# Kernel tuning notes

Hardware: AMD Instinct MI355X
Metric: run time of the kernel (lower is better)

Reference implementation:

```python
import jax, jax.numpy as jnp
import numpy as np

T_SEG = 8      # n_segment
K_SIZE = 3     # dynamic temporal kernel size
BN_EPS = 1e-5


def setup_inputs() -> dict:
    key = jax.random.key(0)
    ks = jax.random.split(key, 8)
    B, T, C, H, W = 8, T_SEG, 256, 56, 56
    ch = C // 4          # c_hidden (reduction=4)
    th = T * 2           # t_hidden (temporal_expand=2)
    K = K_SIZE
    f32 = jnp.float32
    return {
        "x": jax.random.normal(ks[0], (B * T, C, H, W), f32),
        "w_spatial": jax.random.normal(ks[1], (1, 2, 7, 7), f32) * 0.05,   # Conv2d(2,1,7)
        "w_reduce": jax.random.normal(ks[2], (ch, C, 3, 1, 1), f32) * 0.02, # Conv3d(C,ch,(3,1,1))
        "bn_gamma": jnp.ones((ch,), f32),
        "bn_beta": jnp.zeros((ch,), f32),
        "bn_mean": jnp.zeros((ch,), f32),
        "bn_var": jnp.ones((ch,), f32),
        "w_expand": jax.random.normal(ks[3], (C, ch, 1, 1, 1), f32) * 0.02, # Conv3d(ch,C,1)
        "w_fc1": jax.random.normal(ks[4], (th, T), f32) * 0.1,
        "b_fc1": jnp.zeros((th,), f32),
        "w_fc2": jax.random.normal(ks[5], (K, th), f32) * 0.1,
        "b_fc2": jnp.zeros((K,), f32).at[K // 2].set(5.0),
    }


def reference(x, w_spatial, w_reduce, bn_gamma, bn_beta, bn_mean, bn_var,
              w_expand, w_fc1, b_fc1, w_fc2, b_fc2):
    T, K = T_SEG, K_SIZE
    BT, C, H, W = x.shape
    B = BT // T

    # ---- spatial SE gate: channel max/mean -> 7x7 conv -> sigmoid ----
    max_c = x.max(axis=1, keepdims=True)                       # (BT,1,H,W)
    avg_c = x.mean(axis=1, keepdims=True)                      # (BT,1,H,W)
    s = jax.lax.conv_general_dilated(
        jnp.concatenate([max_c, avg_c], axis=1), w_spatial,
        window_strides=(1, 1), padding=((3, 3), (3, 3)),
        dimension_numbers=("NCHW", "OIHW", "NCHW"))
    x_s = x * (1.0 + jax.nn.sigmoid(s))                        # (BT,C,H,W)

    # ---- temporal SE gate: conv3d(3,1,1) -> BN -> relu -> 1x1x1 -> sigmoid ----
    x5 = x_s.reshape(B, T, C, H, W).transpose(0, 2, 1, 3, 4)   # (B,C,T,H,W)
    t = jax.lax.conv_general_dilated(
        x5, w_reduce, window_strides=(1, 1, 1),
        padding=((1, 1), (0, 0), (0, 0)),
        dimension_numbers=("NCDHW", "OIDHW", "NCDHW"))         # (B,ch,T,H,W)
    inv = bn_gamma / jnp.sqrt(bn_var + BN_EPS)
    t = jax.nn.relu(t * inv[None, :, None, None, None]
                    + (bn_beta - bn_mean * inv)[None, :, None, None, None])
    t_attn = jax.nn.sigmoid(
        jnp.einsum("oc,bcthw->bothw", w_expand[:, :, 0, 0, 0], t))
    x_t = x5 * (1.0 + t_attn)                                  # (B,C,T,H,W)

    # ---- dynamic per-(batch,channel) temporal kernel ----
    v = x_t.mean(axis=(-2, -1))                                # (B,C,T)
    h = jax.nn.relu(jnp.einsum("bct,ht->bch", v, w_fc1) + b_fc1)
    kernel = jax.nn.softmax(jnp.einsum("bch,kh->bck", h, w_fc2) + b_fc2,
                            axis=-1)                           # (B,C,K)

    # depthwise temporal stencil (groups=B*C conv2d in torch)
    pad = K // 2
    xp = jnp.pad(x_t, ((0, 0), (0, 0), (pad, pad), (0, 0), (0, 0)))
    out = sum(kernel[:, :, k, None, None, None] * xp[:, :, k:k + T]
              for k in range(K))                               # (B,C,T,H,W)

    return out.transpose(0, 2, 1, 3, 4).reshape(BT, C, H, W)
```

## Files before the change

### kernel.cpp

```cpp
#include <hip/hip_runtime.h>
#include <stdint.h>

#define HW 3136
#define Wd 56
#define Cc 256
#define CH 64
#define Tt 8
#define Bb 8
#define VP 49

typedef unsigned short ushort_t;
typedef __attribute__((ext_vector_type(2))) unsigned short us2;
typedef __attribute__((ext_vector_type(4))) unsigned short us4;
typedef __attribute__((ext_vector_type(8))) unsigned short us8;
typedef __attribute__((ext_vector_type(8))) short short8;
typedef __attribute__((ext_vector_type(4))) float f4;
typedef __attribute__((ext_vector_type(2))) float f2;

__device__ __forceinline__ float bf2f(ushort_t u) {
    union { unsigned int i; float f; } v;
    v.i = ((unsigned int)u) << 16;
    return v.f;
}
__device__ __forceinline__ ushort_t f2bf(float f) {
    union { float f; unsigned int i; } v;
    v.f = f;
    unsigned int r = (v.i + 0x7FFFu + ((v.i >> 16) & 1u)) >> 16;
    return (ushort_t)r;
}

__global__ __launch_bounds__(256) void k0_pack(
    const float* __restrict__ wr, const float* __restrict__ bng,
    const float* __restrict__ bnb, const float* __restrict__ bnm,
    const float* __restrict__ bnv, const float* __restrict__ we,
    ushort_t* __restrict__ wpack, ushort_t* __restrict__ wepack,
    float* __restrict__ shb) {
    int bx = blockIdx.x, tid = threadIdx.x;
    if (bx < 24) {
        int dt = bx >> 3, cb = bx & 7;
        int mt = tid >> 6, l = tid & 63;
        int o = mt * 16 + (l & 15);
        float inv = bng[o] * rsqrtf(bnv[o] + 1e-5f);
        int c0 = cb * 32 + (l >> 4) * 8;
        us8 v;
#pragma unroll
        for (int j = 0; j < 8; j++)
            v[j] = f2bf(wr[((long)o * Cc + c0 + j) * 3 + dt] * inv);
        *(us8*)(wpack + (long)bx * 2048 + (mt * 64 + l) * 8) = v;
        if (bx == 0 && tid < CH)
            shb[tid] = bnb[tid] - bnm[tid] * (bng[tid] * rsqrtf(bnv[tid] + 1e-5f));
    } else {
        int u = (bx - 24) * 256 + tid;
        int l = u & 63;
        int c = ((u >> 6) & 15) * 16 + (l & 15);
        int o0 = (u >> 10) * 32 + (l >> 4) * 8;
        us8 v;
#pragma unroll
        for (int j = 0; j < 8; j++)
            v[j] = f2bf(we[(long)c * CH + o0 + j]);
        *(us8*)(wepack + (long)u * 8) = v;
    }
}

__global__ __launch_bounds__(256) void k1_pool(const float* __restrict__ x,
                                               float* __restrict__ pooled) {
    int u = blockIdx.x * 256 + threadIdx.x;
    int px4 = u % 784, bt = u / 784;
    long base = (long)bt * Cc * HW + px4 * 4;
    float mx[4], sm[4];
#pragma unroll
    for (int j = 0; j < 4; j++) { mx[j] = -3.4e38f; sm[j] = 0.f; }
    for (int c = 0; c < Cc; c++) {
        f4 xv = *(const f4*)(x + base + (long)c * HW);
#pragma unroll
        for (int j = 0; j < 4; j++) {
            mx[j] = fmaxf(mx[j], xv[j]);
            sm[j] += xv[j];
        }
    }
    f4 pm, pa;
#pragma unroll
    for (int j = 0; j < 4; j++) { pm[j] = mx[j]; pa[j] = sm[j] * (1.f / 256.f); }
    *(f4*)(pooled + (long)bt * 2 * HW + px4 * 4) = pm;
    *(f4*)(pooled + (long)bt * 2 * HW + HW + px4 * 4) = pa;
}

__global__ __launch_bounds__(256) void k2_conv(const float* __restrict__ pooled,
                                               const float* __restrict__ wsp,
                                               float* __restrict__ gate) {
    __shared__ float img[2 * HW];
    __shared__ float wf[98];
    int bt = blockIdx.x, tid = threadIdx.x;
    const float* src = pooled + (long)bt * 2 * HW;
    for (int i = tid; i < 2 * HW; i += 256) img[i] = src[i];
    if (tid < 98) wf[tid] = wsp[tid];
    __syncthreads();
    for (int p = tid; p < HW; p += 256) {
        int y = p / Wd, xx = p % Wd;
        float acc = 0.f;
        for (int ci = 0; ci < 2; ci++)
            for (int ky = 0; ky < 7; ky++) {
                int yy = y + ky - 3;
                if (yy < 0 || yy >= Wd) continue;
                for (int kx = 0; kx < 7; kx++) {
                    int xc = xx + kx - 3;
                    if (xc < 0 || xc >= Wd) continue;
                    acc += wf[ci * 49 + ky * 7 + kx] * img[ci * HW + yy * Wd + xc];
                }
            }
        gate[(long)bt * HW + p] = 1.f + 1.f / (1.f + __expf(-acc));
    }
}

__global__ __launch_bounds__(256) void k2t(const float* __restrict__ x,
                                           const float* __restrict__ gate,
                                           ushort_t* __restrict__ xsT) {
    __shared__ __attribute__((aligned(16))) ushort_t lds[64 * 72];
    int tid = threadIdx.x;
    int pblk = blockIdx.x, cblk = blockIdx.y, bt = blockIdx.z;
    int p4 = tid & 15, crow = tid >> 4;
    f4 gv = *(const f4*)(gate + (long)bt * HW + pblk * 64 + p4 * 4);
    long xb = ((long)bt * Cc + cblk * 64 + crow) * HW + pblk * 64 + p4 * 4;
#pragma unroll
    for (int i = 0; i < 4; i++) {
        int c = i * 16 + crow;
        f4 xv = *(const f4*)(x + xb + (long)i * 16 * HW);
#pragma unroll
        for (int k = 0; k < 4; k++) {
            int p = p4 * 4 + k;
            lds[p * 72 + (c ^ (((p >> 3) & 7) * 8))] = f2bf(xv[k] * gv[k]);
        }
    }
    __syncthreads();
    long ob = ((long)bt * HW + pblk * 64) * 256 + cblk * 64;
    int c8 = tid & 7;
#pragma unroll
    for (int j = 0; j < 2; j++) {
        int p = j * 32 + (tid >> 3);
        short8 v = *(const short8*)(&lds[p * 72 + ((c8 * 8) ^ (((p >> 3) & 7) * 8))]);
        *(short8*)(xsT + ob + (long)p * 256 + c8 * 8) = v;
    }
}

__global__ __launch_bounds__(256) void k3m(
    const ushort_t* __restrict__ xsT, const ushort_t* __restrict__ wpack,
    const float* __restrict__ shb, ushort_t* __restrict__ trelu) {
    int l = threadIdx.x;
    int wv = threadIdx.y;
    int bt = blockIdx.y, b = bt >> 3, t = bt & 7;
    int px0 = blockIdx.x * 64 + wv * 16;
    int lr = l & 15, lg = l >> 4;
    f4 acc[4];
#pragma unroll
    for (int mt = 0; mt < 4; mt++)
        acc[mt] = *(const f4*)(shb + mt * 16 + lg * 4);
#pragma unroll
    for (int dt = 0; dt < 3; dt++) {
        int tp = t + dt - 1;
        if (tp < 0 || tp >= Tt) continue;
        const ushort_t* Bp = xsT + ((long)(b * Tt + tp) * HW + px0 + lr) * 256 + lg * 8;
        const ushort_t* Ap = wpack + (long)dt * 8 * 2048 + l * 8;
        for (int cb = 0; cb < 8; cb++) {
            short8 bv = *(const short8*)(Bp + cb * 32);
            const ushort_t* ap = Ap + cb * 2048;
#pragma unroll
            for (int mt = 0; mt < 4; mt++) {
                short8 av = *(const short8*)(ap + mt * 512);
                acc[mt] = __builtin_amdgcn_mfma_f32_16x16x32_bf16(av, bv, acc[mt], 0, 0, 0);
            }
        }
    }
#pragma unroll
    for (int mt = 0; mt < 4; mt++) {
        us4 st;
#pragma unroll
        for (int r = 0; r < 4; r++)
            st[r] = f2bf(fmaxf(acc[mt][r], 0.f));
        *(us4*)(trelu + ((long)bt * HW + px0 + lr) * 64 + mt * 16 + lg * 4) = st;
    }
}

__global__ __launch_bounds__(256) void k4m(
    const float* __restrict__ x, const float* __restrict__ gate,
    const ushort_t* __restrict__ trelu, const ushort_t* __restrict__ wepack,
    ushort_t* __restrict__ xt, float* __restrict__ vpart) {
    int l = threadIdx.x, wv = threadIdx.y;
    int bt = blockIdx.y, b = bt >> 3, t = bt & 7;
    int P0 = blockIdx.x * 64;
    int lr = l & 15, lg = l >> 4;
    int ntg0 = blockIdx.z * 8 + wv * 2;

    short8 bfr[2][2];
#pragma unroll
    for (int kb = 0; kb < 2; kb++)
#pragma unroll
        for (int ni = 0; ni < 2; ni++)
            bfr[kb][ni] = *(const short8*)(wepack + ((long)(kb * 16 + ntg0 + ni) * 64 + l) * 8);

    f4 acc[4][2];
#pragma unroll
    for (int mi = 0; mi < 4; mi++)
#pragma unroll
        for (int ni = 0; ni < 2; ni++) acc[mi][ni] = f4{0.f, 0.f, 0.f, 0.f};

    const ushort_t* Ab = trelu + ((long)bt * HW + P0 + lr) * 64;
#pragma unroll
    for (int mi = 0; mi < 4; mi++) {
#pragma unroll
        for (int kb = 0; kb < 2; kb++) {
            short8 av = *(const short8*)(Ab + (long)mi * 16 * 64 + kb * 32 + lg * 8);
#pragma unroll
            for (int ni = 0; ni < 2; ni++)
                acc[mi][ni] = __builtin_amdgcn_mfma_f32_16x16x32_bf16(av, bfr[kb][ni],
                                                                      acc[mi][ni], 0, 0, 0);
        }
    }

    float csum[2] = {0.f, 0.f};
#pragma unroll
    for (int mi = 0; mi < 4; mi++) {
        int pxb = P0 + mi * 16 + lg * 4;
        f4 gv = *(const f4*)(gate + (long)bt * HW + pxb);
#pragma unroll
        for (int ni = 0; ni < 2; ni++) {
            int c = (ntg0 + ni) * 16 + lr;
            f4 xv = *(const f4*)(x + ((long)bt * Cc + c) * HW + pxb);
            us4 st;
            float s = 0.f;
#pragma unroll
            for (int r = 0; r < 4; r++) {
                float attn = 1.f / (1.f + __expf(-acc[mi][ni][r]));
                float v = xv[r] * gv[r] * (1.f + attn);
                st[r] = f2bf(v);
                s += v;
            }
            *(us4*)(xt + ((long)(b * Cc + c) * Tt + t) * HW + pxb) = st;
            csum[ni] += s;
        }
    }

#pragma unroll
    for (int ni = 0; ni < 2; ni++) {
        float s = csum[ni];
        s += __shfl_xor(s, 16);
        s += __shfl_xor(s, 32);
        if (lg == 0) {
            int c = (ntg0 + ni) * 16 + lr;
            vpart[((long)(b * Cc + c) * Tt + t) * VP + blockIdx.x] = s;
        }
    }
}

__global__ __launch_bounds__(256) void k5_dyn(
    const float* __restrict__ vpart, const float* __restrict__ wfc1,
    const float* __restrict__ bfc1, const float* __restrict__ wfc2,
    const float* __restrict__ bfc2, float* __restrict__ dk) {
    int u = blockIdx.x * 256 + threadIdx.x;
    int b = u >> 8, c = u & 255;
    float v[8];
#pragma unroll
    for (int t = 0; t < 8; t++) {
        float s = 0.f;
        for (int i = 0; i < VP; i++)
            s += vpart[((long)(b * Cc + c) * Tt + t) * VP + i];
        v[t] = s * (1.f / 3136.f);
    }
    float h[16];
#pragma unroll
    for (int j = 0; j < 16; j++) {
        float s = bfc1[j];
        for (int t = 0; t < 8; t++) s += wfc1[j * 8 + t] * v[t];
        h[j] = fmaxf(s, 0.f);
    }
    float l[3];
#pragma unroll
    for (int k = 0; k < 3; k++) {
        float s = bfc2[k];
        for (int j = 0; j < 16; j++) s += wfc2[k * 16 + j] * h[j];
        l[k] = s;
    }
    float m = fmaxf(l[0], fmaxf(l[1], l[2]));
    float e0 = __expf(l[0] - m), e1 = __expf(l[1] - m), e2 = __expf(l[2] - m);
    float inv = 1.f / (e0 + e1 + e2);
    dk[(long)u * 3 + 0] = e0 * inv;
    dk[(long)u * 3 + 1] = e1 * inv;
    dk[(long)u * 3 + 2] = e2 * inv;
}

__global__ __launch_bounds__(256) void k6_stencil(
    const ushort_t* __restrict__ xt, const float* __restrict__ dk,
    float* __restrict__ out) {
    int tx = threadIdx.x;
    int c = blockIdx.y, b = blockIdx.z;
    int px = (blockIdx.x * 256 + tx) * 2;
    if (px >= HW) return;
    const float* kk = dk + (long)(b * Cc + c) * 3;
    float k0 = kk[0], k1 = kk[1], k2 = kk[2];
    float pa[Tt][2];
    const ushort_t* src = xt + (long)(b * Cc + c) * Tt * HW + px;
#pragma unroll
    for (int t = 0; t < Tt; t++) {
        us2 xv = *(const us2*)(src + (long)t * HW);
        pa[t][0] = bf2f(xv[0]);
        pa[t][1] = bf2f(xv[1]);
    }
#pragma unroll
    for (int t = 0; t < Tt; t++) {
        float am = (t > 0) ? pa[t - 1][0] : 0.f, bm = (t > 0) ? pa[t - 1][1] : 0.f;
        float ap = (t < 7) ? pa[t + 1][0] : 0.f, bp = (t < 7) ? pa[t + 1][1] : 0.f;
        f2 r;
        r[0] = k0 * am + k1 * pa[t][0] + k2 * ap;
        r[1] = k0 * bm + k1 * pa[t][1] + k2 * bp;
        *(f2*)(out + ((long)(b * Tt + t) * Cc + c) * HW + px) = r;
    }
}

extern "C" void kernel_launch(void* const* d_in, const int* in_sizes, int n_in,
                              void* d_out, int out_size, void* d_ws, size_t ws_size,
                              hipStream_t stream) {
    const float* x    = (const float*)d_in[0];
    const float* wsp  = (const float*)d_in[1];
    const float* wr   = (const float*)d_in[2];
    const float* bng  = (const float*)d_in[3];
    const float* bnb  = (const float*)d_in[4];
    const float* bnm  = (const float*)d_in[5];
    const float* bnv  = (const float*)d_in[6];
    const float* we   = (const float*)d_in[7];
    const float* wfc1 = (const float*)d_in[8];
    const float* bfc1 = (const float*)d_in[9];
    const float* wfc2 = (const float*)d_in[10];
    const float* bfc2 = (const float*)d_in[11];
    float* out = (float*)d_out;

    char* ws = (char*)d_ws;
    size_t off = 0;
    float* pooled = (float*)(ws + off); off += (size_t)64 * 2 * HW * 4;
    float* gate   = (float*)(ws + off); off += (size_t)64 * HW * 4;
    ushort_t* trelu = (ushort_t*)(ws + off); off += (size_t)Bb * CH * Tt * HW * 2;
    ushort_t* xsT = (ushort_t*)(ws + off); off += (size_t)Bb * Tt * HW * Cc * 2;
    ushort_t* xt = xsT;
    float* vpart  = (float*)(ws + off); off += (size_t)Bb * Cc * Tt * VP * 4;
    float* dk     = (float*)(ws + off); off += (size_t)Bb * Cc * 3 * 4;
    ushort_t* wpack = (ushort_t*)(ws + off); off += (size_t)24 * 2048 * 2;
    ushort_t* wepack = (ushort_t*)(ws + off); off += (size_t)2048 * 8 * 2;
    float* shb    = (float*)(ws + off); off += (size_t)CH * 4;

    hipLaunchKernelGGL(k0_pack, dim3(32), dim3(256), 0, stream,
                       wr, bng, bnb, bnm, bnv, we, wpack, wepack, shb);
    hipLaunchKernelGGL(k1_pool, dim3(196), dim3(256), 0, stream, x, pooled);
    hipLaunchKernelGGL(k2_conv, dim3(64), dim3(256), 0, stream, pooled, wsp, gate);
    hipLaunchKernelGGL(k2t, dim3(49, 4, 64), dim3(256), 0, stream, x, gate, xsT);
    hipLaunchKernelGGL(k3m, dim3(49, 64), dim3(64, 4), 0, stream,
                       xsT, wpack, shb, trelu);
    hipLaunchKernelGGL(k4m, dim3(49, 64, 2), dim3(64, 4), 0, stream,
                       x, gate, trelu, wepack, xt, vpart);
    hipLaunchKernelGGL(k5_dyn, dim3(8), dim3(256), 0, stream,
                       vpart, wfc1, bfc1, wfc2, bfc2, dk);
    hipLaunchKernelGGL(k6_stencil, dim3(7, 256, 8), dim3(256), 0, stream, xt, dk, out);
}
```

Measured before the change: 716.4 us.

## Fuse gating transpose into temporal reduce GEMM, split channel pooling, widen stencil

The gated-x transpose kernel and the temporal-reduce MFMA GEMM become one kernel. It stages gated bf16 activations for all 8 frames of a 32-pixel tile in LDS and runs the 3-tap temporal conv from there, so the full bf16 xsT tensor is no longer written to and re-read from global memory. Channel max/sum pooling is split into 4 channel-quarter blocks for more parallelism, and the conv kernel combines the partials. The stencil now processes 8 pixels per thread with 16-byte loads and stores. The fused kernel uses large blocks and about 37KB of LDS, which may cut occupancy, and pooled partials share workspace with trelu.

```diff
diff --git a/kernel.cpp b/kernel.cpp
--- a/kernel.cpp
+++ b/kernel.cpp
@@ -63,14 +63,15 @@
 }
 
 __global__ __launch_bounds__(256) void k1_pool(const float* __restrict__ x,
-                                               float* __restrict__ pooled) {
+                                               float* __restrict__ pooledp) {
     int u = blockIdx.x * 256 + threadIdx.x;
+    int q = blockIdx.y;
     int px4 = u % 784, bt = u / 784;
-    long base = (long)bt * Cc * HW + px4 * 4;
+    long base = ((long)bt * Cc + (long)q * 64) * HW + px4 * 4;
     float mx[4], sm[4];
 #pragma unroll
     for (int j = 0; j < 4; j++) { mx[j] = -3.4e38f; sm[j] = 0.f; }
-    for (int c = 0; c < Cc; c++) {
+    for (int c = 0; c < 64; c++) {
         f4 xv = *(const f4*)(x + base + (long)c * HW);
 #pragma unroll
         for (int j = 0; j < 4; j++) {
@@ -78,21 +79,30 @@
             sm[j] += xv[j];
         }
     }
-    f4 pm, pa;
-#pragma unroll
-    for (int j = 0; j < 4; j++) { pm[j] = mx[j]; pa[j] = sm[j] * (1.f / 256.f); }
-    *(f4*)(pooled + (long)bt * 2 * HW + px4 * 4) = pm;
-    *(f4*)(pooled + (long)bt * 2 * HW + HW + px4 * 4) = pa;
-}
-
-__global__ __launch_bounds__(256) void k2_conv(const float* __restrict__ pooled,
+    f4 pm, ps;
+#pragma unroll
+    for (int j = 0; j < 4; j++) { pm[j] = mx[j]; ps[j] = sm[j]; }
+    *(f4*)(pooledp + ((long)(q * 64 + bt) * 2 + 0) * HW + px4 * 4) = pm;
+    *(f4*)(pooledp + ((long)(q * 64 + bt) * 2 + 1) * HW + px4 * 4) = ps;
+}
+
+__global__ __launch_bounds__(256) void k2_conv(const float* __restrict__ pooledp,
                                                const float* __restrict__ wsp,
                                                float* __restrict__ gate) {
     __shared__ float img[2 * HW];
     __shared__ float wf[98];
     int bt = blockIdx.x, tid = threadIdx.x;
-    const float* src = pooled + (long)bt * 2 * HW;
-    for (int i = tid; i < 2 * HW; i += 256) img[i] = src[i];
+    for (int i = tid; i < HW; i += 256) {
+        float m = -3.4e38f, s = 0.f;
+#pragma unroll
+        for (int q = 0; q < 4; q++) {
+            const float* pq = pooledp + (long)(q * 64 + bt) * 2 * HW;
+            m = fmaxf(m, pq[i]);
+            s += pq[HW + i];
+        }
+        img[i] = m;
+        img[HW + i] = s * (1.f / 256.f);
+    }
     if (tid < 98) wf[tid] = wsp[tid];
     __syncthreads();
     for (int p = tid; p < HW; p += 256) {
@@ -112,71 +122,82 @@
     }
 }
 
-__global__ __launch_bounds__(256) void k2t(const float* __restrict__ x,
-                                           const float* __restrict__ gate,
-                                           ushort_t* __restrict__ xsT) {
-    __shared__ __attribute__((aligned(16))) ushort_t lds[64 * 72];
+__global__ __launch_bounds__(512) void k23_fused(
+    const float* __restrict__ x, const float* __restrict__ gate,
+    const ushort_t* __restrict__ wpack, const float* __restrict__ shb,
+    ushort_t* __restrict__ trelu) {
+    extern __shared__ char smem[];
+    ushort_t* xs = (ushort_t*)smem;
+    float* gl = (float*)(smem + 256 * 72 * 2);
     int tid = threadIdx.x;
-    int pblk = blockIdx.x, cblk = blockIdx.y, bt = blockIdx.z;
-    int p4 = tid & 15, crow = tid >> 4;
-    f4 gv = *(const f4*)(gate + (long)bt * HW + pblk * 64 + p4 * 4);
-    long xb = ((long)bt * Cc + cblk * 64 + crow) * HW + pblk * 64 + p4 * 4;
-#pragma unroll
-    for (int i = 0; i < 4; i++) {
-        int c = i * 16 + crow;
-        f4 xv = *(const f4*)(x + xb + (long)i * 16 * HW);
-#pragma unroll
-        for (int k = 0; k < 4; k++) {
-            int p = p4 * 4 + k;
-            lds[p * 72 + (c ^ (((p >> 3) & 7) * 8))] = f2bf(xv[k] * gv[k]);
-        }
+    int px0 = blockIdx.x * 32, b = blockIdx.y;
+    if (tid < 256) {
+        int tg = tid >> 5, pg = tid & 31;
+        gl[tid] = gate[(long)(b * 8 + tg) * HW + px0 + pg];
+    }
+    int t = tid >> 6;
+    int l = tid & 63;
+    int lr = l & 15, lg = l >> 4;
+    int cst = tid >> 3;
+    int p4 = tid & 7;
+    f4 acc[4][2];
+#pragma unroll
+    for (int mt = 0; mt < 4; mt++) {
+        f4 bias = *(const f4*)(shb + mt * 16 + lg * 4);
+        acc[mt][0] = bias;
+        acc[mt][1] = bias;
     }
     __syncthreads();
-    long ob = ((long)bt * HW + pblk * 64) * 256 + cblk * 64;
-    int c8 = tid & 7;
-#pragma unroll
-    for (int j = 0; j < 2; j++) {
-        int p = j * 32 + (tid >> 3);
-        short8 v = *(const short8*)(&lds[p * 72 + ((c8 * 8) ^ (((p >> 3) & 7) * 8))]);
-        *(short8*)(xsT + ob + (long)p * 256 + c8 * 8) = v;
-    }
-}
-
-__global__ __launch_bounds__(256) void k3m(
-    const ushort_t* __restrict__ xsT, const ushort_t* __restrict__ wpack,
-    const float* __restrict__ shb, ushort_t* __restrict__ trelu) {
-    int l = threadIdx.x;
-    int wv = threadIdx.y;
-    int bt = blockIdx.y, b = bt >> 3, t = bt & 7;
-    int px0 = blockIdx.x * 64 + wv * 16;
-    int lr = l & 15, lg = l >> 4;
-    f4 acc[4];
-#pragma unroll
-    for (int mt = 0; mt < 4; mt++)
-        acc[mt] = *(const f4*)(shb + mt * 16 + lg * 4);
-#pragma unroll
-    for (int dt = 0; dt < 3; dt++) {
-        int tp = t + dt - 1;
-        if (tp < 0 || tp >= Tt) continue;
-        const ushort_t* Bp = xsT + ((long)(b * Tt + tp) * HW + px0 + lr) * 256 + lg * 8;
-        const ushort_t* Ap = wpack + (long)dt * 8 * 2048 + l * 8;
-        for (int cb = 0; cb < 8; cb++) {
-            short8 bv = *(const short8*)(Bp + cb * 32);
-            const ushort_t* ap = Ap + cb * 2048;
-#pragma unroll
-            for (int mt = 0; mt < 4; mt++) {
-                short8 av = *(const short8*)(ap + mt * 512);
-                acc[mt] = __builtin_amdgcn_mfma_f32_16x16x32_bf16(av, bv, acc[mt], 0, 0, 0);
+    for (int ch = 0; ch < 4; ch++) {
+#pragma unroll
+        for (int tt = 0; tt < 8; tt++) {
+            f4 xv = *(const f4*)(x + ((long)(b * 8 + tt) * Cc + ch * 64 + cst) * HW
+                                 + px0 + p4 * 4);
+            const float* gp = gl + tt * 32 + p4 * 4;
+#pragma unroll
+            for (int k = 0; k < 4; k++) {
+                int p = p4 * 4 + k;
+                xs[(tt * 32 + p) * 72 + (cst ^ (((p >> 3) & 7) * 8))] = f2bf(xv[k] * gp[k]);
             }
         }
-    }
-#pragma unroll
-    for (int mt = 0; mt < 4; mt++) {
-        us4 st;
-#pragma unroll
-        for (int r = 0; r < 4; r++)
-            st[r] = f2bf(fmaxf(acc[mt][r], 0.f));
-        *(us4*)(trelu + ((long)bt * HW + px0 + lr) * 64 + mt * 16 + lg * 4) = st;
+        __syncthreads();
+#pragma unroll
+        for (int dt = 0; dt < 3; dt++) {
+            int tp = t + dt - 1;
+            if (tp >= 0 && tp < Tt) {
+                const ushort_t* Ap = wpack + ((long)(dt * 8 + ch * 2)) * 2048 + l * 8;
+#pragma unroll
+                for (int kb = 0; kb < 2; kb++) {
+                    short8 av[4];
+#pragma unroll
+                    for (int mt = 0; mt < 4; mt++)
+                        av[mt] = *(const short8*)(Ap + kb * 2048 + mt * 512);
+#pragma unroll
+                    for (int nt = 0; nt < 2; nt++) {
+                        int pxl = nt * 16 + lr;
+                        short8 bv = *(const short8*)(&xs[(tp * 32 + pxl) * 72 +
+                                        ((kb * 32 + lg * 8) ^ (((pxl >> 3) & 7) * 8))]);
+#pragma unroll
+                        for (int mt = 0; mt < 4; mt++)
+                            acc[mt][nt] = __builtin_amdgcn_mfma_f32_16x16x32_bf16(
+                                av[mt], bv, acc[mt][nt], 0, 0, 0);
+                    }
+                }
+            }
+        }
+        __syncthreads();
+    }
+#pragma unroll
+    for (int nt = 0; nt < 2; nt++) {
+#pragma unroll
+        for (int mt = 0; mt < 4; mt++) {
+            us4 st;
+#pragma unroll
+            for (int r = 0; r < 4; r++)
+                st[r] = f2bf(fmaxf(acc[mt][nt][r], 0.f));
+            *(us4*)(trelu + ((long)(b * 8 + t) * HW + px0 + nt * 16 + lr) * 64
+                    + mt * 16 + lg * 4) = st;
+        }
     }
 }
 
@@ -290,28 +311,38 @@
 __global__ __launch_bounds__(256) void k6_stencil(
     const ushort_t* __restrict__ xt, const float* __restrict__ dk,
     float* __restrict__ out) {
-    int tx = threadIdx.x;
-    int c = blockIdx.y, b = blockIdx.z;
-    int px = (blockIdx.x * 256 + tx) * 2;
-    if (px >= HW) return;
-    const float* kk = dk + (long)(b * Cc + c) * 3;
+    int u = blockIdx.x * 256 + threadIdx.x;
+    int px8 = u % 392, bc = u / 392;
+    int px = px8 * 8;
+    const float* kk = dk + (long)bc * 3;
     float k0 = kk[0], k1 = kk[1], k2 = kk[2];
-    float pa[Tt][2];
-    const ushort_t* src = xt + (long)(b * Cc + c) * Tt * HW + px;
+    float pa[Tt][8];
+    const ushort_t* src = xt + (long)bc * Tt * HW + px;
 #pragma unroll
     for (int t = 0; t < Tt; t++) {
-        us2 xv = *(const us2*)(src + (long)t * HW);
-        pa[t][0] = bf2f(xv[0]);
-        pa[t][1] = bf2f(xv[1]);
-    }
+        us8 xv = *(const us8*)(src + (long)t * HW);
+#pragma unroll
+        for (int j = 0; j < 8; j++) pa[t][j] = bf2f(xv[j]);
+    }
+    int c = bc & 255, b = bc >> 8;
 #pragma unroll
     for (int t = 0; t < Tt; t++) {
-        float am = (t > 0) ? pa[t - 1][0] : 0.f, bm = (t > 0) ? pa[t - 1][1] : 0.f;
-        float ap = (t < 7) ? pa[t + 1][0] : 0.f, bp = (t < 7) ? pa[t + 1][1] : 0.f;
-        f2 r;
-        r[0] = k0 * am + k1 * pa[t][0] + k2 * ap;
-        r[1] = k0 * bm + k1 * pa[t][1] + k2 * bp;
-        *(f2*)(out + ((long)(b * Tt + t) * Cc + c) * HW + px) = r;
+        f4 r0, r1;
+#pragma unroll
+        for (int j = 0; j < 4; j++) {
+            float m = (t > 0) ? pa[t - 1][j] : 0.f;
+            float p = (t < 7) ? pa[t + 1][j] : 0.f;
+            r0[j] = k0 * m + k1 * pa[t][j] + k2 * p;
+        }
+#pragma unroll
+        for (int j = 0; j < 4; j++) {
+            float m = (t > 0) ? pa[t - 1][4 + j] : 0.f;
+            float p = (t < 7) ? pa[t + 1][4 + j] : 0.f;
+            r1[j] = k0 * m + k1 * pa[t][4 + j] + k2 * p;
+        }
+        float* op = out + ((long)(b * Tt + t) * Cc + c) * HW + px;
+        *(f4*)(op) = r0;
+        *(f4*)(op + 4) = r1;
     }
 }
 
@@ -334,11 +365,10 @@
 
     char* ws = (char*)d_ws;
     size_t off = 0;
-    float* pooled = (float*)(ws + off); off += (size_t)64 * 2 * HW * 4;
+    ushort_t* trelu = (ushort_t*)(ws + off); off += (size_t)Bb * CH * Tt * HW * 2;
+    float* pooledp = (float*)trelu;
     float* gate   = (float*)(ws + off); off += (size_t)64 * HW * 4;
-    ushort_t* trelu = (ushort_t*)(ws + off); off += (size_t)Bb * CH * Tt * HW * 2;
-    ushort_t* xsT = (ushort_t*)(ws + off); off += (size_t)Bb * Tt * HW * Cc * 2;
-    ushort_t* xt = xsT;
+    ushort_t* xt  = (ushort_t*)(ws + off); off += (size_t)Bb * Cc * Tt * HW * 2;
     float* vpart  = (float*)(ws + off); off += (size_t)Bb * Cc * Tt * VP * 4;
     float* dk     = (float*)(ws + off); off += (size_t)Bb * Cc * 3 * 4;
     ushort_t* wpack = (ushort_t*)(ws + off); off += (size_t)24 * 2048 * 2;
@@ -347,14 +377,13 @@
 
     hipLaunchKernelGGL(k0_pack, dim3(32), dim3(256), 0, stream,
                        wr, bng, bnb, bnm, bnv, we, wpack, wepack, shb);
-    hipLaunchKernelGGL(k1_pool, dim3(196), dim3(256), 0, stream, x, pooled);
-    hipLaunchKernelGGL(k2_conv, dim3(64), dim3(256), 0, stream, pooled, wsp, gate);
-    hipLaunchKernelGGL(k2t, dim3(49, 4, 64), dim3(256), 0, stream, x, gate, xsT);
-    hipLaunchKernelGGL(k3m, dim3(49, 64), dim3(64, 4), 0, stream,
-                       xsT, wpack, shb, trelu);
+    hipLaunchKernelGGL(k1_pool, dim3(196, 4), dim3(256), 0, stream, x, pooledp);
+    hipLaunchKernelGGL(k2_conv, dim3(64), dim3(256), 0, stream, pooledp, wsp, gate);
+    hipLaunchKernelGGL(k23_fused, dim3(98, 8), dim3(512), 37888, stream,
+                       x, gate, wpack, shb, trelu);
     hipLaunchKernelGGL(k4m, dim3(49, 64, 2), dim3(64, 4), 0, stream,
                        x, gate, trelu, wepack, xt, vpart);
     hipLaunchKernelGGL(k5_dyn, dim3(8), dim3(256), 0, stream,
                        vpart, wfc1, bfc1, wfc2, bfc2, dk);
-    hipLaunchKernelGGL(k6_stencil, dim3(7, 256, 8), dim3(256), 0, stream, xt, dk, out);
-}
+    hipLaunchKernelGGL(k6_stencil, dim3(3136), dim3(256), 0, stream, xt, dk, out);
+}
```

New measurement: 663.1 us. 7.4% less time.
